# Kernel tuning notes

Measured on AMD Instinct MI355X. Metric: run time of the kernel, lower is better.

## Reference

```python
import jax, jax.numpy as jnp
import numpy as np

B, T, L, H = 16, 16, 512, 768


def setup_inputs() -> dict:
    key = jax.random.key(0)
    k1, k2, k3, k4, k5, k6 = jax.random.split(key, 6)
    hn = jax.random.normal(k1, (B, L, H), dtype=jnp.float32)
    decoder_out = jax.random.normal(k2, (B, L, H), dtype=jnp.float32)
    W1 = jax.random.normal(k3, (H, H), dtype=jnp.float32) * (1.0 / np.sqrt(H))
    W2 = jax.random.normal(k4, (H, H), dtype=jnp.float32) * (1.0 / np.sqrt(H))
    V = jax.random.normal(k5, (H,), dtype=jnp.float32) * (1.0 / np.sqrt(H))
    # Ragged, consistent pointer indices: T monotone segment starts per sample,
    # gold boundary Yindex[b,t] in [Xindex[b,t], L).
    step = L // T  # 32
    Xindex = jnp.broadcast_to(jnp.arange(T, dtype=jnp.int64) * step, (B, T))
    offsets = jax.random.randint(k6, (B, T), 0, step, dtype=jnp.int64)
    Yindex = Xindex + offsets
    lens = jnp.full((B,), L, dtype=jnp.int64)
    return {"hn": hn, "decoder_out": decoder_out, "W1": W1, "W2": W2, "V": V,
            "Xindex": Xindex, "Yindex": Yindex, "lens": lens}


def reference(hn, decoder_out, W1, W2, V, Xindex, Yindex, lens):
    # Faithful batched form of training_decoder + pointerLayer:
    #   for each sample i, step j:
    #     en = hn[i, Xindex[i,j]:lens[i]]            (ragged suffix)
    #     dj = decoder_out[i, Yindex[i,j]]           (cur_dj = decoder_out[cur_groundy])
    #     s  = selu(V @ selu(W1 en + W2 dj))
    #     loss += NLL(log_softmax(s), Yindex[i,j]-Xindex[i,j])
    WE = jnp.einsum('blh,gh->blg', hn, W1)                        # [B,L,H]  nnW1(en)
    dj = jnp.take_along_axis(decoder_out, Yindex[:, :, None], axis=1)  # [B,T,H]
    WD = jnp.einsum('bth,gh->btg', dj, W2)                        # [B,T,H]  nnW2(dj)
    act = jax.nn.selu(WE[:, None, :, :] + WD[:, :, None, :])      # [B,T,L,H]
    scores = jax.nn.selu(jnp.einsum('btlh,h->btl', act, V))       # [B,T,L]
    pos = jnp.arange(hn.shape[1])
    mask = (pos[None, None, :] >= Xindex[:, :, None]) & (pos[None, None, :] < lens[:, None, None])
    neg_inf = jnp.finfo(scores.dtype).min
    masked = jnp.where(mask, scores, neg_inf)
    logp = masked - jax.scipy.special.logsumexp(masked, axis=-1, keepdims=True)
    # logits index (Yindex - Xindex) in the sliced array == global index Yindex
    gold = jnp.take_along_axis(logp, Yindex[:, :, None], axis=-1)[..., 0]  # [B,T]
    return -jnp.mean(gold)
```

## Files before the change

### kernel.cpp

```cpp
#include <hip/hip_runtime.h>
#include <hip/hip_bf16.h>
#include <math.h>

#define SELU_SCALE 1.0507009873554805f
#define SELU_ALPHA 1.6732632423543772f

static constexpr int B_ = 16, T_ = 16, L_ = 512, H_ = 768;
static constexpr int WSZ = 768 * 768;

typedef __bf16 bf16x8 __attribute__((ext_vector_type(8)));
typedef float  f32x4  __attribute__((ext_vector_type(4)));

__device__ __forceinline__ float bf_lo(unsigned u) { return __uint_as_float(u << 16); }
__device__ __forceinline__ float bf_hi(unsigned u) { return __uint_as_float(u & 0xFFFF0000u); }

__device__ __forceinline__ float selu_core(float x) {
    float e = fmaf(__expf(x), SELU_ALPHA, -SELU_ALPHA);
    return x > 0.0f ? x : e;
}

__device__ __forceinline__ int xsw(int r) { return (r >> 1) & 3; }

__device__ __forceinline__ bf16x8 pack8(float4 a, float4 b) {
    bf16x8 o;
    o[0] = (__bf16)a.x; o[1] = (__bf16)a.y; o[2] = (__bf16)a.z; o[3] = (__bf16)a.w;
    o[4] = (__bf16)b.x; o[5] = (__bf16)b.y; o[6] = (__bf16)b.z; o[7] = (__bf16)b.w;
    return o;
}

__global__ __launch_bounds__(256) void prep_k(
        const float* __restrict__ w1, const float* __restrict__ w2,
        __bf16* __restrict__ wb, float* __restrict__ out) {
    if (blockIdx.x == 0 && threadIdx.x == 0) out[0] = 0.0f;
    int idx = (blockIdx.x * 256 + threadIdx.x) * 8;
    const float* src = idx < WSZ ? w1 + idx : w2 + (idx - WSZ);
    float4 a = *(const float4*)src;
    float4 b = *(const float4*)(src + 4);
    *(bf16x8*)(wb + idx) = pack8(a, b);
}

__global__ __launch_bounds__(256, 2) void gemm_k(
        const float* __restrict__ hn, const float* __restrict__ dec,
        const __bf16* __restrict__ wb, const int* __restrict__ Yi,
        __bf16* __restrict__ web, float* __restrict__ wdf) {
    __shared__ __bf16 As[128 * 32];

    const int tid = threadIdx.x;

    int bx = blockIdx.x;
    const __bf16* Wb; int m0, n0; bool wd;
    if (bx < 384) {
        wd = false; Wb = wb;
        m0 = (bx & 63) * 128; n0 = (bx >> 6) * 128;
    } else {
        wd = true; bx -= 384; Wb = wb + WSZ;
        m0 = (bx & 1) * 128;  n0 = (bx >> 1) * 128;
    }

    const int wave = tid >> 6, lane = tid & 63;
    const int wm = (wave >> 1) * 64, wn = (wave & 1) * 64;
    const int lr = lane & 15, q = lane >> 4;

    const int r1 = wave * 32 + (lane >> 2);
    const int s3 = lane & 3;
    const int g1 = s3 ^ xsw(r1);

    const float *aG1, *aG2;
    if (!wd) {
        aG1 = hn + (size_t)(m0 + r1) * 768 + g1 * 8;
        aG2 = aG1 + (size_t)16 * 768;
    } else {
        int bt1 = m0 + r1, bt2 = bt1 + 16;
        aG1 = dec + ((size_t)((bt1 >> 4) * L_ + Yi[bt1])) * 768 + g1 * 8;
        aG2 = dec + ((size_t)((bt2 >> 4) * L_ + Yi[bt2])) * 768 + g1 * 8;
    }

    bf16x8* AsW1 = (bf16x8*)&As[r1 * 32 + s3 * 8];
    bf16x8* AsW2 = (bf16x8*)&As[(r1 + 16) * 32 + s3 * 8];

    int aoff[4];
#pragma unroll
    for (int i = 0; i < 4; ++i) {
        int r = wm + i * 16 + lr;
        aoff[i] = r * 32 + (q ^ xsw(r)) * 8;
    }

    const __bf16* pB = Wb + (size_t)(n0 + wn + lr) * 768 + q * 8;

    f32x4 acc[4][4] = {};

    float4 xa1a = *(const float4*)(aG1);      float4 xa1b = *(const float4*)(aG1 + 4);
    float4 xa2a = *(const float4*)(aG2);      float4 xa2b = *(const float4*)(aG2 + 4);
    float4 ya1a = *(const float4*)(aG1 + 32); float4 ya1b = *(const float4*)(aG1 + 36);
    float4 ya2a = *(const float4*)(aG2 + 32); float4 ya2b = *(const float4*)(aG2 + 36);

    bf16x8 bX[4], bY[4];
#pragma unroll
    for (int j = 0; j < 4; ++j) bX[j] = *(const bf16x8*)(pB + j * 12288);

#pragma unroll 1
    for (int k0 = 0; k0 < 768; k0 += 64) {
        {
            *AsW1 = pack8(xa1a, xa1b);
            *AsW2 = pack8(xa2a, xa2b);
            asm volatile("s_waitcnt lgkmcnt(0)\n\ts_barrier" ::: "memory");
            if (k0 + 64 < 768) {
                xa1a = *(const float4*)(aG1 + k0 + 64); xa1b = *(const float4*)(aG1 + k0 + 68);
                xa2a = *(const float4*)(aG2 + k0 + 64); xa2b = *(const float4*)(aG2 + k0 + 68);
            }
#pragma unroll
            for (int j = 0; j < 4; ++j)
                bY[j] = *(const bf16x8*)(pB + j * 12288 + k0 + 32);
            bf16x8 af[4];
#pragma unroll
            for (int i = 0; i < 4; ++i) af[i] = *(const bf16x8*)&As[aoff[i]];
#pragma unroll
            for (int i = 0; i < 4; ++i)
#pragma unroll
                for (int j = 0; j < 4; ++j)
                    acc[i][j] = __builtin_amdgcn_mfma_f32_16x16x32_bf16(af[i], bX[j], acc[i][j], 0, 0, 0);
            asm volatile("s_barrier" ::: "memory");
        }
        {
            *AsW1 = pack8(ya1a, ya1b);
            *AsW2 = pack8(ya2a, ya2b);
            asm volatile("s_waitcnt lgkmcnt(0)\n\ts_barrier" ::: "memory");
            if (k0 + 96 < 768) {
                ya1a = *(const float4*)(aG1 + k0 + 96); ya1b = *(const float4*)(aG1 + k0 + 100);
                ya2a = *(const float4*)(aG2 + k0 + 96); ya2b = *(const float4*)(aG2 + k0 + 100);
            }
            if (k0 + 64 < 768) {
#pragma unroll
                for (int j = 0; j < 4; ++j)
                    bX[j] = *(const bf16x8*)(pB + j * 12288 + k0 + 64);
            }
            bf16x8 af[4];
#pragma unroll
            for (int i = 0; i < 4; ++i) af[i] = *(const bf16x8*)&As[aoff[i]];
#pragma unroll
            for (int i = 0; i < 4; ++i)
#pragma unroll
                for (int j = 0; j < 4; ++j)
                    acc[i][j] = __builtin_amdgcn_mfma_f32_16x16x32_bf16(af[i], bY[j], acc[i][j], 0, 0, 0);
            asm volatile("s_barrier" ::: "memory");
        }
    }

#pragma unroll
    for (int i = 0; i < 4; ++i)
#pragma unroll
        for (int j = 0; j < 4; ++j)
#pragma unroll
            for (int r = 0; r < 4; ++r) {
                int row = m0 + wm + i * 16 + q * 4 + r;
                int col = n0 + wn + j * 16 + lr;
                if (!wd) web[(size_t)row * 768 + col] = (__bf16)acc[i][j][r];
                else     wdf[(size_t)row * 768 + col] = acc[i][j][r];
            }
}

__global__ __launch_bounds__(256, 4) void scores_k(
        const __bf16* __restrict__ web, const float* __restrict__ wdf,
        const float* __restrict__ V, const int* __restrict__ Xi,
        float* __restrict__ scores) {
    const int b  = blockIdx.x;
    const int l0 = ((int)gridDim.y - 1 - (int)blockIdx.y) * 16;
    const int t0 = blockIdx.z * 8;
    const int tid = threadIdx.x;
    const int ls = tid >> 4, hc = tid & 15;
    const int l  = l0 + ls;
    const int h0 = hc * 8;

    float we[48], vv[48];
    const __bf16* wr = web + ((size_t)(b * L_ + l)) * H_ + h0;
#pragma unroll
    for (int j = 0; j < 6; ++j) {
        uint4 u = *(const uint4*)(wr + j * 128);
        we[j*8+0] = bf_lo(u.x); we[j*8+1] = bf_hi(u.x);
        we[j*8+2] = bf_lo(u.y); we[j*8+3] = bf_hi(u.y);
        we[j*8+4] = bf_lo(u.z); we[j*8+5] = bf_hi(u.z);
        we[j*8+6] = bf_lo(u.w); we[j*8+7] = bf_hi(u.w);
    }
    const float* vp = V + h0;
#pragma unroll
    for (int j = 0; j < 6; ++j) {
        float4 a = *(const float4*)(vp + j * 128);
        float4 c = *(const float4*)(vp + j * 128 + 4);
        vv[j*8+0] = a.x; vv[j*8+1] = a.y; vv[j*8+2] = a.z; vv[j*8+3] = a.w;
        vv[j*8+4] = c.x; vv[j*8+5] = c.y; vv[j*8+6] = c.z; vv[j*8+7] = c.w;
    }

    const int wmaxl = l0 + ((tid >> 6) << 2) + 3;
    const int bT = b * T_;
#pragma unroll 1
    for (int t = t0; t < t0 + 8; ++t) {
        const int X = Xi[bT + t];
        if (wmaxl < X) continue;
        const float* wdp = wdf + ((size_t)(bT + t)) * H_ + h0;
        float a0 = 0.f, a1 = 0.f, a2 = 0.f, a3 = 0.f;
#pragma unroll
        for (int j = 0; j < 6; ++j) {
            float4 x = *(const float4*)(wdp + j * 128);
            float4 y = *(const float4*)(wdp + j * 128 + 4);
            a0 = fmaf(selu_core(we[j*8+0] + x.x), vv[j*8+0], a0);
            a1 = fmaf(selu_core(we[j*8+1] + x.y), vv[j*8+1], a1);
            a2 = fmaf(selu_core(we[j*8+2] + x.z), vv[j*8+2], a2);
            a3 = fmaf(selu_core(we[j*8+3] + x.w), vv[j*8+3], a3);
            a0 = fmaf(selu_core(we[j*8+4] + y.x), vv[j*8+4], a0);
            a1 = fmaf(selu_core(we[j*8+5] + y.y), vv[j*8+5], a1);
            a2 = fmaf(selu_core(we[j*8+6] + y.z), vv[j*8+6], a2);
            a3 = fmaf(selu_core(we[j*8+7] + y.w), vv[j*8+7], a3);
        }
        float dot = (a0 + a1) + (a2 + a3);
        dot += __shfl_xor(dot, 1);
        dot += __shfl_xor(dot, 2);
        dot += __shfl_xor(dot, 4);
        dot += __shfl_xor(dot, 8);
        if (hc == 0) {
            dot *= SELU_SCALE;
            float sc = dot > 0.0f ? SELU_SCALE * dot
                                  : SELU_SCALE * SELU_ALPHA * (__expf(dot) - 1.0f);
            scores[((size_t)(bT + t)) * L_ + l] = sc;
        }
    }
}

__global__ __launch_bounds__(64) void loss_k(
        const float* __restrict__ scores, const int* __restrict__ Xi,
        const int* __restrict__ Yi, float* __restrict__ out) {
    const int bt = blockIdx.x;
    const int lane = threadIdx.x;
    const int X = Xi[bt];
    const int Y = Yi[bt];
    const float* row = scores + (size_t)bt * L_;

    float m = -INFINITY;
    for (int l = X + lane; l < L_; l += 64) m = fmaxf(m, row[l]);
#pragma unroll
    for (int off = 32; off > 0; off >>= 1) m = fmaxf(m, __shfl_xor(m, off));

    float s = 0.0f;
    for (int l = X + lane; l < L_; l += 64) s += __expf(row[l] - m);
#pragma unroll
    for (int off = 32; off > 0; off >>= 1) s += __shfl_xor(s, off);

    if (lane == 0)
        atomicAdd(out, (m + __logf(s) - row[Y]) * (1.0f / (B_ * T_)));
}

extern "C" void kernel_launch(void* const* d_in, const int* in_sizes, int n_in,
                              void* d_out, int out_size, void* d_ws, size_t ws_size,
                              hipStream_t stream) {
    const float* hn  = (const float*)d_in[0];
    const float* dec = (const float*)d_in[1];
    const float* W1  = (const float*)d_in[2];
    const float* W2  = (const float*)d_in[3];
    const float* V   = (const float*)d_in[4];
    const int*   Xi  = (const int*)d_in[5];
    const int*   Yi  = (const int*)d_in[6];
    float* out = (float*)d_out;

    char* ws = (char*)d_ws;
    size_t off = 0;
    auto alloc = [&](size_t bytes) -> char* {
        char* p = ws + off;
        off += (bytes + 255) & ~(size_t)255;
        return p;
    };
    __bf16* web    = (__bf16*)alloc((size_t)B_ * L_ * H_ * 2);
    float*  wdf    = (float*)alloc((size_t)B_ * T_ * H_ * 4);
    float*  scores = (float*)alloc((size_t)B_ * T_ * L_ * 4);
    __bf16* wb     = (__bf16*)alloc((size_t)2 * WSZ * 2);

    prep_k<<<2 * WSZ / (256 * 8), 256, 0, stream>>>(W1, W2, wb, out);
    gemm_k<<<396, 256, 0, stream>>>(hn, dec, wb, Yi, web, wdf);
    scores_k<<<dim3(B_, L_ / 16, 2), 256, 0, stream>>>(web, wdf, V, Xi, scores);
    loss_k<<<B_ * T_, 64, 0, stream>>>(scores, Xi, Yi, out);
}
```

Before: 161.8 us.

## Pre-convert hn and gathered decoder rows to bf16, drop LDS staging in GEMM

The prep kernel now converts hn, W1, W2 and the Yindex-gathered decoder rows into one contiguous bf16 buffer. The GEMM then loads both A and B fragments directly from global memory into registers with a three-stage register pipeline, removing the shared-memory tile, packing and barriers. This halves the bytes the GEMM reads for A but adds a full extra pass over hn (fp32 read plus bf16 write) in the prep kernel. A fragments are no longer shared across waves, so the GEMM issues more redundant global/L2 loads.

```diff
diff --git a/kernel.cpp b/kernel.cpp
--- a/kernel.cpp
+++ b/kernel.cpp
@@ -7,6 +7,9 @@
 
 static constexpr int B_ = 16, T_ = 16, L_ = 512, H_ = 768;
 static constexpr int WSZ = 768 * 768;
+static constexpr int HNELEM = B_ * L_ * H_;
+static constexpr int DJELEM = B_ * T_ * H_;
+static constexpr int ALLELEM = HNELEM + 2 * WSZ + DJELEM;
 
 typedef __bf16 bf16x8 __attribute__((ext_vector_type(8)));
 typedef float  f32x4  __attribute__((ext_vector_type(4)));
@@ -18,8 +21,6 @@
     float e = fmaf(__expf(x), SELU_ALPHA, -SELU_ALPHA);
     return x > 0.0f ? x : e;
 }
-
-__device__ __forceinline__ int xsw(int r) { return (r >> 1) & 3; }
 
 __device__ __forceinline__ bf16x8 pack8(float4 a, float4 b) {
     bf16x8 o;
@@ -29,122 +30,84 @@
 }
 
 __global__ __launch_bounds__(256) void prep_k(
+        const float* __restrict__ hn, const float* __restrict__ dec,
         const float* __restrict__ w1, const float* __restrict__ w2,
-        __bf16* __restrict__ wb, float* __restrict__ out) {
+        const int* __restrict__ Yi,
+        __bf16* __restrict__ allb, float* __restrict__ out) {
     if (blockIdx.x == 0 && threadIdx.x == 0) out[0] = 0.0f;
     int idx = (blockIdx.x * 256 + threadIdx.x) * 8;
-    const float* src = idx < WSZ ? w1 + idx : w2 + (idx - WSZ);
+    const float* src;
+    if (idx < HNELEM) {
+        src = hn + idx;
+    } else if (idx < HNELEM + WSZ) {
+        src = w1 + (idx - HNELEM);
+    } else if (idx < HNELEM + 2 * WSZ) {
+        src = w2 + (idx - HNELEM - WSZ);
+    } else {
+        int e = idx - (HNELEM + 2 * WSZ);
+        int r = e / 768, c = e - r * 768;
+        src = dec + ((size_t)((r >> 4) * L_ + Yi[r])) * H_ + c;
+    }
     float4 a = *(const float4*)src;
     float4 b = *(const float4*)(src + 4);
-    *(bf16x8*)(wb + idx) = pack8(a, b);
+    *(bf16x8*)(allb + idx) = pack8(a, b);
 }
 
 __global__ __launch_bounds__(256, 2) void gemm_k(
-        const float* __restrict__ hn, const float* __restrict__ dec,
-        const __bf16* __restrict__ wb, const int* __restrict__ Yi,
+        const __bf16* __restrict__ allb,
         __bf16* __restrict__ web, float* __restrict__ wdf) {
-    __shared__ __bf16 As[128 * 32];
-
-    const int tid = threadIdx.x;
-
     int bx = blockIdx.x;
-    const __bf16* Wb; int m0, n0; bool wd;
+    const __bf16 *Ab, *Bb; int m0, n0; bool wd;
     if (bx < 384) {
-        wd = false; Wb = wb;
+        wd = false; Ab = allb; Bb = allb + HNELEM;
         m0 = (bx & 63) * 128; n0 = (bx >> 6) * 128;
     } else {
-        wd = true; bx -= 384; Wb = wb + WSZ;
+        wd = true; bx -= 384; Ab = allb + HNELEM + 2 * WSZ; Bb = allb + HNELEM + WSZ;
         m0 = (bx & 1) * 128;  n0 = (bx >> 1) * 128;
     }
 
-    const int wave = tid >> 6, lane = tid & 63;
+    const int tid = threadIdx.x, wave = tid >> 6, lane = tid & 63;
     const int wm = (wave >> 1) * 64, wn = (wave & 1) * 64;
     const int lr = lane & 15, q = lane >> 4;
 
-    const int r1 = wave * 32 + (lane >> 2);
-    const int s3 = lane & 3;
-    const int g1 = s3 ^ xsw(r1);
-
-    const float *aG1, *aG2;
-    if (!wd) {
-        aG1 = hn + (size_t)(m0 + r1) * 768 + g1 * 8;
-        aG2 = aG1 + (size_t)16 * 768;
-    } else {
-        int bt1 = m0 + r1, bt2 = bt1 + 16;
-        aG1 = dec + ((size_t)((bt1 >> 4) * L_ + Yi[bt1])) * 768 + g1 * 8;
-        aG2 = dec + ((size_t)((bt2 >> 4) * L_ + Yi[bt2])) * 768 + g1 * 8;
-    }
-
-    bf16x8* AsW1 = (bf16x8*)&As[r1 * 32 + s3 * 8];
-    bf16x8* AsW2 = (bf16x8*)&As[(r1 + 16) * 32 + s3 * 8];
-
-    int aoff[4];
-#pragma unroll
-    for (int i = 0; i < 4; ++i) {
-        int r = wm + i * 16 + lr;
-        aoff[i] = r * 32 + (q ^ xsw(r)) * 8;
-    }
-
-    const __bf16* pB = Wb + (size_t)(n0 + wn + lr) * 768 + q * 8;
+    const __bf16* pA[4]; const __bf16* pB[4];
+#pragma unroll
+    for (int i = 0; i < 4; ++i) pA[i] = Ab + (size_t)(m0 + wm + i * 16 + lr) * 768 + q * 8;
+#pragma unroll
+    for (int j = 0; j < 4; ++j) pB[j] = Bb + (size_t)(n0 + wn + j * 16 + lr) * 768 + q * 8;
 
     f32x4 acc[4][4] = {};
-
-    float4 xa1a = *(const float4*)(aG1);      float4 xa1b = *(const float4*)(aG1 + 4);
-    float4 xa2a = *(const float4*)(aG2);      float4 xa2b = *(const float4*)(aG2 + 4);
-    float4 ya1a = *(const float4*)(aG1 + 32); float4 ya1b = *(const float4*)(aG1 + 36);
-    float4 ya2a = *(const float4*)(aG2 + 32); float4 ya2b = *(const float4*)(aG2 + 36);
-
-    bf16x8 bX[4], bY[4];
-#pragma unroll
-    for (int j = 0; j < 4; ++j) bX[j] = *(const bf16x8*)(pB + j * 12288);
+    bf16x8 a0v[4], b0v[4], a1v[4], b1v[4], a2v[4], b2v[4];
+
+#pragma unroll
+    for (int i = 0; i < 4; ++i) { a0v[i] = *(const bf16x8*)(pA[i]);      b0v[i] = *(const bf16x8*)(pB[i]); }
+#pragma unroll
+    for (int i = 0; i < 4; ++i) { a1v[i] = *(const bf16x8*)(pA[i] + 32); b1v[i] = *(const bf16x8*)(pB[i] + 32); }
+
+#define PHASE(SA, SB, LA, LB, KL)                                              \
+    {                                                                          \
+        if ((KL) < 768) {                                                      \
+            _Pragma("unroll")                                                  \
+            for (int i = 0; i < 4; ++i) {                                      \
+                LA[i] = *(const bf16x8*)(pA[i] + (KL));                        \
+                LB[i] = *(const bf16x8*)(pB[i] + (KL));                        \
+            }                                                                  \
+        }                                                                      \
+        _Pragma("unroll")                                                      \
+        for (int i = 0; i < 4; ++i)                                            \
+            _Pragma("unroll")                                                  \
+            for (int j = 0; j < 4; ++j)                                        \
+                acc[i][j] = __builtin_amdgcn_mfma_f32_16x16x32_bf16(           \
+                    SA[i], SB[j], acc[i][j], 0, 0, 0);                         \
+    }
 
 #pragma unroll 1
-    for (int k0 = 0; k0 < 768; k0 += 64) {
-        {
-            *AsW1 = pack8(xa1a, xa1b);
-            *AsW2 = pack8(xa2a, xa2b);
-            asm volatile("s_waitcnt lgkmcnt(0)\n\ts_barrier" ::: "memory");
-            if (k0 + 64 < 768) {
-                xa1a = *(const float4*)(aG1 + k0 + 64); xa1b = *(const float4*)(aG1 + k0 + 68);
-                xa2a = *(const float4*)(aG2 + k0 + 64); xa2b = *(const float4*)(aG2 + k0 + 68);
-            }
-#pragma unroll
-            for (int j = 0; j < 4; ++j)
-                bY[j] = *(const bf16x8*)(pB + j * 12288 + k0 + 32);
-            bf16x8 af[4];
-#pragma unroll
-            for (int i = 0; i < 4; ++i) af[i] = *(const bf16x8*)&As[aoff[i]];
-#pragma unroll
-            for (int i = 0; i < 4; ++i)
-#pragma unroll
-                for (int j = 0; j < 4; ++j)
-                    acc[i][j] = __builtin_amdgcn_mfma_f32_16x16x32_bf16(af[i], bX[j], acc[i][j], 0, 0, 0);
-            asm volatile("s_barrier" ::: "memory");
-        }
-        {
-            *AsW1 = pack8(ya1a, ya1b);
-            *AsW2 = pack8(ya2a, ya2b);
-            asm volatile("s_waitcnt lgkmcnt(0)\n\ts_barrier" ::: "memory");
-            if (k0 + 96 < 768) {
-                ya1a = *(const float4*)(aG1 + k0 + 96); ya1b = *(const float4*)(aG1 + k0 + 100);
-                ya2a = *(const float4*)(aG2 + k0 + 96); ya2b = *(const float4*)(aG2 + k0 + 100);
-            }
-            if (k0 + 64 < 768) {
-#pragma unroll
-                for (int j = 0; j < 4; ++j)
-                    bX[j] = *(const bf16x8*)(pB + j * 12288 + k0 + 64);
-            }
-            bf16x8 af[4];
-#pragma unroll
-            for (int i = 0; i < 4; ++i) af[i] = *(const bf16x8*)&As[aoff[i]];
-#pragma unroll
-            for (int i = 0; i < 4; ++i)
-#pragma unroll
-                for (int j = 0; j < 4; ++j)
-                    acc[i][j] = __builtin_amdgcn_mfma_f32_16x16x32_bf16(af[i], bY[j], acc[i][j], 0, 0, 0);
-            asm volatile("s_barrier" ::: "memory");
-        }
-    }
+    for (int k0 = 0; k0 < 768; k0 += 96) {
+        PHASE(a0v, b0v, a2v, b2v, k0 + 64)
+        PHASE(a1v, b1v, a0v, b0v, k0 + 96)
+        PHASE(a2v, b2v, a1v, b1v, k0 + 128)
+    }
+#undef PHASE
 
 #pragma unroll
     for (int i = 0; i < 4; ++i)
@@ -270,10 +233,10 @@
     __bf16* web    = (__bf16*)alloc((size_t)B_ * L_ * H_ * 2);
     float*  wdf    = (float*)alloc((size_t)B_ * T_ * H_ * 4);
     float*  scores = (float*)alloc((size_t)B_ * T_ * L_ * 4);
-    __bf16* wb     = (__bf16*)alloc((size_t)2 * WSZ * 2);
-
-    prep_k<<<2 * WSZ / (256 * 8), 256, 0, stream>>>(W1, W2, wb, out);
-    gemm_k<<<396, 256, 0, stream>>>(hn, dec, wb, Yi, web, wdf);
+    __bf16* allb   = (__bf16*)alloc((size_t)ALLELEM * 2);
+
+    prep_k<<<ALLELEM / (256 * 8), 256, 0, stream>>>(hn, dec, W1, W2, Yi, allb, out);
+    gemm_k<<<396, 256, 0, stream>>>(allb, web, wdf);
     scores_k<<<dim3(B_, L_ / 16, 2), 256, 0, stream>>>(web, wdf, V, Xi, scores);
     loss_k<<<B_ * T_, 64, 0, stream>>>(scores, Xi, Yi, out);
 }
```

Measured after the change: 176.8 us. +9.3%, slower.
